# Kernel tuning notes

Hardware: AMD Instinct MI355X
Metric: run time of the kernel (lower is better)

The kernel has to match this reference:

```python
import jax, jax.numpy as jnp
import numpy as np

EPS = 1e-8

def real_sph_harm(u):
    # u: [..., 3] unit vectors; returns real spherical harmonics for degrees 0..3
    x, y, z = u[..., 0], u[..., 1], u[..., 2]
    x2, y2, z2 = x * x, y * y, z * z
    Y0 = 0.28209479 * jnp.ones_like(x)[..., None]                       # [..., 1]
    Y1 = 0.48860251 * jnp.stack([y, z, x], axis=-1)                     # [..., 3]
    Y2 = jnp.stack([
        1.09254843 * x * y,
        1.09254843 * y * z,
        0.31539157 * (3.0 * z2 - 1.0),
        1.09254843 * x * z,
        0.54627422 * (x2 - y2)], axis=-1)                               # [..., 5]
    Y3 = jnp.stack([
        0.59004359 * y * (3.0 * x2 - y2),
        2.89061144 * x * y * z,
        0.45704579 * y * (5.0 * z2 - 1.0),
        0.37317633 * z * (5.0 * z2 - 3.0),
        0.45704579 * x * (5.0 * z2 - 1.0),
        1.44530572 * z * (x2 - y2),
        0.59004359 * x * (x2 - 3.0 * y2)], axis=-1)                     # [..., 7]
    return [Y0, Y1, Y2, Y3]


def setup_inputs() -> dict:
    key = jax.random.key(0)
    ks = jax.random.split(key, 8)
    B, N, F_IN, C, L = 8, 256, 4, 32, 4
    F_OUT = L * C * 2  # 256
    D_OUT = 40
    H = 32  # radial MLP hidden
    s = 0.1
    return {
        "x": jax.random.normal(ks[0], (B, N, F_IN), jnp.float32),
        "Wq": jax.random.normal(ks[1], (F_IN, C), jnp.float32) * s,
        "Wk": jax.random.normal(ks[2], (F_IN, C), jnp.float32) * s,
        "Wv": jax.random.normal(ks[3], (L, F_IN, C), jnp.float32) * s,
        "Rw1": jax.random.normal(ks[4], (1, H), jnp.float32) * s,
        "Rb1": jnp.zeros((H,), jnp.float32),
        "Rw2": jax.random.normal(ks[5], (H, L * C), jnp.float32) * s,
        "Rb2": jnp.zeros((L * C,), jnp.float32),
        "fc1_w": jax.random.normal(ks[6], (F_OUT, F_OUT), jnp.float32) * s,
        "fc1_b": jnp.zeros((F_OUT,), jnp.float32),
        "ln_g": jnp.ones((F_OUT,), jnp.float32),
        "ln_b": jnp.zeros((F_OUT,), jnp.float32),
        "fc2_w": jax.random.normal(ks[7], (F_OUT, D_OUT), jnp.float32) * s,
        "fc2_b": jnp.zeros((D_OUT,), jnp.float32),
    }


def reference(x, Wq, Wk, Wv, Rw1, Rb1, Rw2, Rb2, fc1_w, fc1_b, ln_g, ln_b, fc2_w, fc2_b):
    B, N, _ = x.shape
    L, _, C = Wv.shape
    # --- basis and r (get_basis_and_r): all-pairs displacements from coords ---
    coords = x[..., :3]
    d = coords[:, None, :, :] - coords[:, :, None, :]          # [B, i, j, 3]
    r = jnp.sqrt(jnp.sum(d * d, axis=-1) + EPS)                # [B, i, j]
    u = d / r[..., None]
    Ys = real_sph_harm(u)                                      # list of [B,i,j,2l+1]
    # --- radial net: per-degree, per-channel radial weights ---
    h = jax.nn.relu(r[..., None] @ Rw1 + Rb1)                  # [B,i,j,H]
    R = (h @ Rw2 + Rb2).reshape(B, N, N, L, C)                 # [B,i,j,L,C]
    # --- SSO3Res: equivariant attention (degree-0 q/k, basis-weighted values) ---
    q = x @ Wq
    k = x @ Wk
    logits = jnp.einsum('bic,bjc->bij', q, k) / jnp.sqrt(jnp.asarray(C, x.dtype))
    alpha = jax.nn.softmax(logits, axis=-1)                    # [B,i,j]
    vals = jnp.einsum('bjf,lfc->lbjc', x, Wv)                  # [L,B,j,C]
    invs = []
    for l in range(L):
        # out_l[i,c,m] = sum_j alpha_ij * R_ij,c * Y_l,ij,m * v_j,c
        out_l = jnp.einsum('bij,bijc,bijm,bjc->bicm', alpha, R[..., l, :], Ys[l], vals[l])
        invs.append(jnp.sqrt(jnp.sum(out_l * out_l, axis=-1) + EPS))   # [B,i,C]
    inv = jnp.concatenate(invs, axis=-1)                       # [B, N, L*C]
    # --- invariant pooling: max + mean over points -> out fiber (L*C*2) ---
    pooled = jnp.concatenate([inv.max(axis=1), inv.mean(axis=1)], axis=-1)  # [B, 2*L*C]
    # --- FC head: Linear -> LayerNorm -> ReLU -> Linear ---
    h1 = pooled @ fc1_w + fc1_b
    mu = h1.mean(axis=-1, keepdims=True)
    var = h1.var(axis=-1, keepdims=True)
    h1 = (h1 - mu) / jnp.sqrt(var + 1e-5) * ln_g + ln_b
    h1 = jax.nn.relu(h1)
    return h1 @ fc2_w + fc2_b
```

## Files before the change

### kernel.cpp

```cpp
#include <hip/hip_runtime.h>
#include <hip/hip_bf16.h>

#define BB 8
#define NN 256
#define LC 128

typedef short short8 __attribute__((ext_vector_type(8)));
typedef float f32x4 __attribute__((ext_vector_type(4)));

union U8 { short8 s; unsigned u[4]; };

__device__ inline unsigned pkbf(float a, float b){
    __hip_bfloat162 h = __float22bfloat162_rn(make_float2(a, b));
    union { __hip_bfloat162 h2; unsigned u; } cv; cv.h2 = h; return cv.u;
}

__device__ inline void stage_aY(short* __restrict__ slab, int j, float a,
                                float dx, float dy, float dz, float r2)
{
    const float ir = rsqrtf(r2);
    const float ux = dx*ir, uy = dy*ir, uz = dz*ir;
    const float X2 = ux*ux, Y2 = uy*uy, Z2 = uz*uz;
    const float y0  = 0.28209479f;
    const float y1  = 0.48860251f*uy, y2 = 0.48860251f*uz, y3 = 0.48860251f*ux;
    const float y4  = 1.09254843f*ux*uy;
    const float y5  = 1.09254843f*uy*uz;
    const float y6  = 0.31539157f*(3.f*Z2 - 1.f);
    const float y7  = 1.09254843f*ux*uz;
    const float y8  = 0.54627422f*(X2 - Y2);
    const float y9  = 0.59004359f*uy*(3.f*X2 - Y2);
    const float y10 = 2.89061144f*ux*uy*uz;
    const float y11 = 0.45704579f*uy*(5.f*Z2 - 1.f);
    const float y12 = 0.37317633f*uz*(5.f*Z2 - 3.f);
    const float y13 = 0.45704579f*ux*(5.f*Z2 - 1.f);
    const float y14 = 1.44530572f*uz*(X2 - Y2);
    const float y15 = 0.59004359f*ux*(X2 - 3.f*Y2);
    #define ST2(mm, va, vb) { unsigned uu = pkbf((va)*a, (vb)*a); \
        slab[(mm)*264 + j] = (short)(uu & 0xffff); slab[(mm+1)*264 + j] = (short)(uu >> 16); }
    ST2(0,  y0,  y1)  ST2(2,  y2,  y3)
    ST2(4,  y4,  y5)  ST2(6,  y6,  y7)
    ST2(8,  y8,  y9)  ST2(10, y10, y11)
    ST2(12, y12, y13) ST2(14, y14, y15)
    #undef ST2
}

__global__ __launch_bounds__(256) void so3_main(
    const float* __restrict__ xg,
    const float* __restrict__ Wq,
    const float* __restrict__ Wk,
    const float* __restrict__ Wv,
    const float* __restrict__ Rw1,
    const float* __restrict__ Rb1,
    const float* __restrict__ Rw2,
    const float* __restrict__ Rb2,
    float* __restrict__ invg)
{
    const int tid = threadIdx.x;
    const int blk = blockIdx.x;
    const int b = blk >> 6;
    const int iq = blk & 63;
    const int rowbase = b * NN;
    const int lane = tid & 63;
    const int w = tid >> 6;
    const int n = lane & 15;
    const int g = lane >> 4;
    const int kbase = g * 8;
    const int i = iq*4 + w;

    __shared__ __align__(16) float xs[NN*4];
    __shared__ short xsbf[NN*4];
    __shared__ short aYs[4][16*264];
    __shared__ float asum[4][256];

    const float4 x4 = *(const float4*)&xg[(rowbase + tid)*4];
    *(float4*)&xs[tid*4] = x4;
    {
        uint2 xb;
        xb.x = pkbf(x4.x, x4.y);
        xb.y = pkbf(x4.z, x4.w);
        *(uint2*)&xsbf[tid*4] = xb;
    }
    const float4 xi = *(const float4*)&xg[(rowbase + i)*4];

    float md0, md1, md2, md3;
    {
        const int c = lane & 31;
        const float qc = xi.x*Wq[c] + xi.y*Wq[32+c] + xi.z*Wq[64+c] + xi.w*Wq[96+c];
        md0 = qc*Wk[c]; md1 = qc*Wk[32+c]; md2 = qc*Wk[64+c]; md3 = qc*Wk[96+c];
        #pragma unroll
        for (int off = 16; off >= 1; off >>= 1) {
            md0 += __shfl_xor(md0, off);
            md1 += __shfl_xor(md1, off);
            md2 += __shfl_xor(md2, off);
            md3 += __shfl_xor(md3, off);
        }
        const float lscale = 0.17677669529663687f;
        md0 *= lscale; md1 *= lscale; md2 *= lscale; md3 *= lscale;
    }

    __syncthreads();

    float r_reg[16], lgv[16];
    #pragma unroll
    for (int s = 0; s < 16; ++s) {
        const float4 xa = *(const float4*)&xs[(16*s + n)*4];
        const float ddx = xa.x - xi.x, ddy = xa.y - xi.y, ddz = xa.z - xi.z;
        const float r2 = ddx*ddx + ddy*ddy + ddz*ddz + 1e-8f;
        r_reg[s] = sqrtf(r2);
        lgv[s] = md0*xa.x + md1*xa.y + md2*xa.z + md3*xa.w;
    }

    float mx = lgv[0];
    #pragma unroll
    for (int s = 1; s < 16; ++s) mx = fmaxf(mx, lgv[s]);
    #pragma unroll
    for (int off = 1; off <= 8; off <<= 1) mx = fmaxf(mx, __shfl_xor(mx, off));
    float es = 0.f;
    float ev[16];
    #pragma unroll
    for (int s = 0; s < 16; ++s) { ev[s] = __expf(lgv[s] - mx); es += ev[s]; }
    #pragma unroll
    for (int off = 1; off <= 8; off <<= 1) es += __shfl_xor(es, off);
    const float invS = 1.0f / es;
    #pragma unroll
    for (int s = 0; s < 16; ++s) asum[w][16*s + n] = ev[s]*invS;

    asm volatile("s_waitcnt lgkmcnt(0)" ::: "memory");
    __builtin_amdgcn_sched_barrier(0);

    short* slab = &aYs[w][0];
    #pragma unroll
    for (int e = 0; e < 4; ++e) {
        const int j = 64*g + 16*e + n;
        const float a = asum[w][j];
        const float4 xa = *(const float4*)&xs[j*4];
        const float ddx = xa.x - xi.x, ddy = xa.y - xi.y, ddz = xa.z - xi.z;
        const float r2 = ddx*ddx + ddy*ddy + ddz*ddz + 1e-8f;
        stage_aY(slab, j, a, ddx, ddy, ddz, r2);
    }

    float rw1q[8], rb1q[8];
    #pragma unroll
    for (int q = 0; q < 8; ++q) { rw1q[q] = Rw1[kbase+q]; rb1q[q] = Rb1[kbase+q]; }

    asm volatile("s_waitcnt lgkmcnt(0)" ::: "memory");
    __builtin_amdgcn_sched_barrier(0);

    const int boff = n*264 + 4*g;
    const f32x4 vzero = {0.f, 0.f, 0.f, 0.f};

    #pragma unroll
    for (int h4 = 0; h4 < 2; ++h4) {
        short8 bfrag[4], bv[4];
        float rb2v[4];
        #pragma unroll
        for (int t4 = 0; t4 < 4; ++t4) {
            const int col = h4*64 + t4*16 + n;
            U8 bf;
            #pragma unroll
            for (int qq = 0; qq < 4; ++qq)
                bf.u[qq] = pkbf(Rw2[(kbase+2*qq)*LC + col], Rw2[(kbase+2*qq+1)*LC + col]);
            bfrag[t4] = bf.s;
            rb2v[t4] = Rb2[col];
            U8 z; z.u[0] = 0; z.u[1] = 0; z.u[2] = 0; z.u[3] = 0;
            if (g == 0) {
                const int l = (h4*64 + t4*16) >> 5;
                const int cc = (t4 & 1)*16 + n;
                z.u[0] = pkbf(Wv[l*128 + cc],      Wv[l*128 + 32 + cc]);
                z.u[1] = pkbf(Wv[l*128 + 64 + cc], Wv[l*128 + 96 + cc]);
            }
            bv[t4] = z.s;
        }

        f32x4 acc[4] = {};

        #pragma unroll
        for (int tt = 0; tt < 8; ++tt) {
            const int j0 = 32*tt;

            const uint2 blo = *(const uint2*)&slab[boff + j0];
            const uint2 bhi = *(const uint2*)&slab[boff + j0 + 16];
            U8 bf2;
            bf2.u[0] = blo.x; bf2.u[1] = blo.y; bf2.u[2] = bhi.x; bf2.u[3] = bhi.y;

            uint2 P[2][4];
            #pragma unroll
            for (int jh = 0; jh < 2; ++jh) {
                const float rj = r_reg[2*tt + jh];
                U8 af;
                #pragma unroll
                for (int qq = 0; qq < 4; ++qq) {
                    const float h0 = fmaxf(rj*rw1q[2*qq]   + rb1q[2*qq],   0.f);
                    const float h1 = fmaxf(rj*rw1q[2*qq+1] + rb1q[2*qq+1], 0.f);
                    af.u[qq] = pkbf(h0, h1);
                }
                U8 afV; afV.u[0] = 0; afV.u[1] = 0; afV.u[2] = 0; afV.u[3] = 0;
                if (g == 0) {
                    const uint2 xb = *(const uint2*)&xsbf[(j0 + 16*jh + n)*4];
                    afV.u[0] = xb.x; afV.u[1] = xb.y;
                }
                #pragma unroll
                for (int t4 = 0; t4 < 4; ++t4) {
                    f32x4 d  = __builtin_amdgcn_mfma_f32_16x16x32_bf16(af.s,  bfrag[t4], vzero, 0, 0, 0);
                    f32x4 vv = __builtin_amdgcn_mfma_f32_16x16x32_bf16(afV.s, bv[t4],    vzero, 0, 0, 0);
                    P[jh][t4].x = pkbf((d[0]+rb2v[t4])*vv[0], (d[1]+rb2v[t4])*vv[1]);
                    P[jh][t4].y = pkbf((d[2]+rb2v[t4])*vv[2], (d[3]+rb2v[t4])*vv[3]);
                }
            }

            #pragma unroll
            for (int t4 = 0; t4 < 4; ++t4) {
                U8 a2;
                a2.u[0] = P[0][t4].x; a2.u[1] = P[0][t4].y;
                a2.u[2] = P[1][t4].x; a2.u[3] = P[1][t4].y;
                acc[t4] = __builtin_amdgcn_mfma_f32_16x16x32_bf16(a2.s, bf2.s, acc[t4], 0, 0, 0);
            }
        }

        #pragma unroll
        for (int t4 = 0; t4 < 4; ++t4) {
            const int l = h4*2 + (t4 >> 1);
            const int lo = l*l, hi = l*l + 2*l;
            const bool valid = (n >= lo) && (n <= hi);
            f32x4 aq = acc[t4];
            float s0 = valid ? aq[0]*aq[0] : 0.f;
            float s1 = valid ? aq[1]*aq[1] : 0.f;
            float s2 = valid ? aq[2]*aq[2] : 0.f;
            float s3 = valid ? aq[3]*aq[3] : 0.f;
            #pragma unroll
            for (int off = 1; off <= 8; off <<= 1) {
                s0 += __shfl_xor(s0, off);
                s1 += __shfl_xor(s1, off);
                s2 += __shfl_xor(s2, off);
                s3 += __shfl_xor(s3, off);
            }
            const float sv = (n==0) ? s0 : ((n==1) ? s1 : ((n==2) ? s2 : s3));
            if (n < 4) asum[w][h4*64 + t4*16 + g*4 + n] = sv;
        }
    }

    asm volatile("s_waitcnt lgkmcnt(0)" ::: "memory");
    __builtin_amdgcn_sched_barrier(0);
    {
        const float v0 = asum[w][lane];
        const float v1 = asum[w][lane + 64];
        float* dst = &invg[(size_t)(rowbase + i)*LC];
        dst[lane]      = sqrtf(v0 + 1e-8f);
        dst[lane + 64] = sqrtf(v1 + 1e-8f);
    }
}

__global__ __launch_bounds__(1024) void so3_post(
    const float* __restrict__ invg,
    const float* __restrict__ fc1_w,
    const float* __restrict__ fc1_b,
    const float* __restrict__ ln_g,
    const float* __restrict__ ln_b,
    const float* __restrict__ fc2_w,
    const float* __restrict__ fc2_b,
    float* __restrict__ outg)
{
    const int b = blockIdx.x;
    const int t = threadIdx.x;
    __shared__ float pm[8][128], ps[8][128];
    __shared__ float pooled[256];
    __shared__ float pfc1[2][256];
    __shared__ float h1s[256];
    __shared__ float pf2[8][40];
    __shared__ float redA[4], redB[4];

    {
        const int ig = t >> 7, lc = t & 127;
        float mxv = -1e30f, sm = 0.f;
        for (int i2 = ig; i2 < NN; i2 += 8) {
            const float v = invg[(size_t)(b*NN + i2)*LC + lc];
            mxv = fmaxf(mxv, v);
            sm += v;
        }
        pm[ig][lc] = mxv; ps[ig][lc] = sm;
    }
    __syncthreads();
    if (t < 128) {
        float m0 = pm[0][t];
        #pragma unroll
        for (int k = 1; k < 8; ++k) m0 = fmaxf(m0, pm[k][t]);
        pooled[t] = m0;
    } else if (t < 256) {
        const int lc = t - 128;
        float s0 = ps[0][lc];
        #pragma unroll
        for (int k = 1; k < 8; ++k) s0 += ps[k][lc];
        pooled[t] = s0 * (1.f/256.f);
    }
    __syncthreads();

    if (t < 512) {
        const int o = t & 255, kh = t >> 8;
        float acc = 0.f;
        for (int k = kh*128; k < kh*128 + 128; ++k)
            acc += pooled[k] * fc1_w[k*256 + o];
        pfc1[kh][o] = acc;
    }
    __syncthreads();

    float hval = 0.f;
    if (t < 256) hval = pfc1[0][t] + pfc1[1][t] + fc1_b[t];

    const int lane = t & 63, wid = t >> 6;
    float s1 = (t < 256) ? hval : 0.f;
    float s2 = (t < 256) ? hval*hval : 0.f;
    #pragma unroll
    for (int off = 32; off >= 1; off >>= 1) {
        s1 += __shfl_xor(s1, off);
        s2 += __shfl_xor(s2, off);
    }
    if (lane == 0 && wid < 4) { redA[wid] = s1; redB[wid] = s2; }
    __syncthreads();
    s1 = redA[0]+redA[1]+redA[2]+redA[3];
    s2 = redB[0]+redB[1]+redB[2]+redB[3];
    if (t < 256) {
        const float mu = s1 * (1.f/256.f);
        const float var = s2 * (1.f/256.f) - mu*mu;
        float v = (hval - mu) * rsqrtf(var + 1e-5f) * ln_g[t] + ln_b[t];
        h1s[t] = fmaxf(v, 0.f);
    }
    __syncthreads();

    if (t < 320) {
        const int o = t % 40, ks = t / 40;
        float acc = 0.f;
        for (int k = ks*32; k < ks*32 + 32; ++k)
            acc += h1s[k] * fc2_w[k*40 + o];
        pf2[ks][o] = acc;
    }
    __syncthreads();
    if (t < 40) {
        float o = fc2_b[t];
        #pragma unroll
        for (int ks = 0; ks < 8; ++ks) o += pf2[ks][t];
        outg[b*40 + t] = o;
    }
}

extern "C" void kernel_launch(void* const* d_in, const int* in_sizes, int n_in,
                              void* d_out, int out_size, void* d_ws, size_t ws_size,
                              hipStream_t stream) {
    const float* x     = (const float*)d_in[0];
    const float* Wq    = (const float*)d_in[1];
    const float* Wk    = (const float*)d_in[2];
    const float* Wv    = (const float*)d_in[3];
    const float* Rw1   = (const float*)d_in[4];
    const float* Rb1   = (const float*)d_in[5];
    const float* Rw2   = (const float*)d_in[6];
    const float* Rb2   = (const float*)d_in[7];
    const float* fc1_w = (const float*)d_in[8];
    const float* fc1_b = (const float*)d_in[9];
    const float* ln_g  = (const float*)d_in[10];
    const float* ln_b  = (const float*)d_in[11];
    const float* fc2_w = (const float*)d_in[12];
    const float* fc2_b = (const float*)d_in[13];
    float* out = (float*)d_out;

    float* invg = (float*)d_ws;

    so3_main<<<BB*64, 256, 0, stream>>>(x, Wq, Wk, Wv, Rw1, Rb1, Rw2, Rb2, invg);
    so3_post<<<BB, 1024, 0, stream>>>(invg, fc1_w, fc1_b, ln_g, ln_b, fc2_w, fc2_b, out);
}
```

Before: 43.43 us.

## Split rows across wave pairs, prepack weights, pool via atomics

```diff
diff --git a/kernel.cpp b/kernel.cpp
--- a/kernel.cpp
+++ b/kernel.cpp
@@ -44,33 +44,67 @@
     #undef ST2
 }
 
+__global__ __launch_bounds__(256) void so3_init(
+    const float* __restrict__ Rw2,
+    const float* __restrict__ Wv,
+    float* __restrict__ pmaxg,
+    float* __restrict__ psumg,
+    short* __restrict__ RW2bf,
+    short* __restrict__ WvBbf)
+{
+    const int t = threadIdx.x;
+    #pragma unroll
+    for (int rr = 0; rr < 4; ++rr) {
+        pmaxg[rr*256 + t] = 0.f;
+        psumg[rr*256 + t] = 0.f;
+    }
+    {
+        const int col = t >> 1, kh = (t & 1) * 16;
+        unsigned uu[8];
+        #pragma unroll
+        for (int q = 0; q < 8; ++q)
+            uu[q] = pkbf(Rw2[(kh + 2*q)*LC + col], Rw2[(kh + 2*q + 1)*LC + col]);
+        *(uint4*)&RW2bf[col*32 + kh]     = make_uint4(uu[0], uu[1], uu[2], uu[3]);
+        *(uint4*)&RW2bf[col*32 + kh + 8] = make_uint4(uu[4], uu[5], uu[6], uu[7]);
+    }
+    if (t < 128) {
+        const int l = t >> 5, c = t & 31;
+        const unsigned a0 = pkbf(Wv[l*128 + c],      Wv[l*128 + 32 + c]);
+        const unsigned a1 = pkbf(Wv[l*128 + 64 + c], Wv[l*128 + 96 + c]);
+        *(uint2*)&WvBbf[t*4] = make_uint2(a0, a1);
+    }
+}
+
 __global__ __launch_bounds__(256) void so3_main(
     const float* __restrict__ xg,
     const float* __restrict__ Wq,
     const float* __restrict__ Wk,
-    const float* __restrict__ Wv,
     const float* __restrict__ Rw1,
     const float* __restrict__ Rb1,
-    const float* __restrict__ Rw2,
+    const short* __restrict__ RW2bf,
     const float* __restrict__ Rb2,
-    float* __restrict__ invg)
+    const short* __restrict__ WvBbf,
+    float* __restrict__ pmaxg,
+    float* __restrict__ psumg)
 {
     const int tid = threadIdx.x;
     const int blk = blockIdx.x;
-    const int b = blk >> 6;
-    const int iq = blk & 63;
+    const int b = blk >> 7;
+    const int i0 = (blk & 127) << 1;
     const int rowbase = b * NN;
     const int lane = tid & 63;
     const int w = tid >> 6;
+    const int iw = w >> 1;
+    const int h = w & 1;
     const int n = lane & 15;
     const int g = lane >> 4;
     const int kbase = g * 8;
-    const int i = iq*4 + w;
+    const int i = i0 + iw;
 
     __shared__ __align__(16) float xs[NN*4];
     __shared__ short xsbf[NN*4];
-    __shared__ short aYs[4][16*264];
-    __shared__ float asum[4][256];
+    __shared__ short slab2[2][16*264];
+    __shared__ float aex[2][NN];
 
     const float4 x4 = *(const float4*)&xg[(rowbase + tid)*4];
     *(float4*)&xs[tid*4] = x4;
@@ -115,143 +149,127 @@
     for (int s = 1; s < 16; ++s) mx = fmaxf(mx, lgv[s]);
     #pragma unroll
     for (int off = 1; off <= 8; off <<= 1) mx = fmaxf(mx, __shfl_xor(mx, off));
-    float es = 0.f;
-    float ev[16];
+    float ev[16], es = 0.f;
     #pragma unroll
     for (int s = 0; s < 16; ++s) { ev[s] = __expf(lgv[s] - mx); es += ev[s]; }
     #pragma unroll
     for (int off = 1; off <= 8; off <<= 1) es += __shfl_xor(es, off);
     const float invS = 1.0f / es;
     #pragma unroll
-    for (int s = 0; s < 16; ++s) asum[w][16*s + n] = ev[s]*invS;
+    for (int s = 0; s < 16; ++s) aex[iw][16*s + n] = ev[s]*invS;
 
     asm volatile("s_waitcnt lgkmcnt(0)" ::: "memory");
     __builtin_amdgcn_sched_barrier(0);
 
-    short* slab = &aYs[w][0];
-    #pragma unroll
-    for (int e = 0; e < 4; ++e) {
-        const int j = 64*g + 16*e + n;
-        const float a = asum[w][j];
+    short* sl = &slab2[iw][0];
+    #pragma unroll
+    for (int e = 0; e < 2; ++e) {
+        const int j = 128*h + 16*(2*g + e) + n;
+        const float a = aex[iw][j];
         const float4 xa = *(const float4*)&xs[j*4];
         const float ddx = xa.x - xi.x, ddy = xa.y - xi.y, ddz = xa.z - xi.z;
         const float r2 = ddx*ddx + ddy*ddy + ddz*ddz + 1e-8f;
-        stage_aY(slab, j, a, ddx, ddy, ddz, r2);
+        stage_aY(sl, j, a, ddx, ddy, ddz, r2);
     }
 
     float rw1q[8], rb1q[8];
     #pragma unroll
     for (int q = 0; q < 8; ++q) { rw1q[q] = Rw1[kbase+q]; rb1q[q] = Rb1[kbase+q]; }
 
-    asm volatile("s_waitcnt lgkmcnt(0)" ::: "memory");
-    __builtin_amdgcn_sched_barrier(0);
+    short8 bfrag[4], bv[4];
+    float rb2v[4];
+    #pragma unroll
+    for (int t4 = 0; t4 < 4; ++t4) {
+        const int col = h*64 + t4*16 + n;
+        bfrag[t4] = *(const short8*)&RW2bf[col*32 + kbase];
+        rb2v[t4] = Rb2[col];
+        U8 z; z.u[0] = 0; z.u[1] = 0; z.u[2] = 0; z.u[3] = 0;
+        if (g == 0) {
+            const uint2 f = *(const uint2*)&WvBbf[col*4];
+            z.u[0] = f.x; z.u[1] = f.y;
+        }
+        bv[t4] = z.s;
+    }
+
+    __syncthreads();
 
     const int boff = n*264 + 4*g;
     const f32x4 vzero = {0.f, 0.f, 0.f, 0.f};
-
-    #pragma unroll
-    for (int h4 = 0; h4 < 2; ++h4) {
-        short8 bfrag[4], bv[4];
-        float rb2v[4];
-        #pragma unroll
-        for (int t4 = 0; t4 < 4; ++t4) {
-            const int col = h4*64 + t4*16 + n;
-            U8 bf;
+    f32x4 acc[4] = {};
+
+    #pragma unroll
+    for (int tt = 0; tt < 8; ++tt) {
+        const int j0 = 32*tt;
+
+        const uint2 blo = *(const uint2*)&sl[boff + j0];
+        const uint2 bhi = *(const uint2*)&sl[boff + j0 + 16];
+        U8 bf2;
+        bf2.u[0] = blo.x; bf2.u[1] = blo.y; bf2.u[2] = bhi.x; bf2.u[3] = bhi.y;
+
+        uint2 P[2][4];
+        #pragma unroll
+        for (int jh = 0; jh < 2; ++jh) {
+            const float rj = r_reg[2*tt + jh];
+            U8 af;
             #pragma unroll
-            for (int qq = 0; qq < 4; ++qq)
-                bf.u[qq] = pkbf(Rw2[(kbase+2*qq)*LC + col], Rw2[(kbase+2*qq+1)*LC + col]);
-            bfrag[t4] = bf.s;
-            rb2v[t4] = Rb2[col];
-            U8 z; z.u[0] = 0; z.u[1] = 0; z.u[2] = 0; z.u[3] = 0;
+            for (int qq = 0; qq < 4; ++qq) {
+                const float h0 = fmaxf(rj*rw1q[2*qq]   + rb1q[2*qq],   0.f);
+                const float h1 = fmaxf(rj*rw1q[2*qq+1] + rb1q[2*qq+1], 0.f);
+                af.u[qq] = pkbf(h0, h1);
+            }
+            U8 afV; afV.u[0] = 0; afV.u[1] = 0; afV.u[2] = 0; afV.u[3] = 0;
             if (g == 0) {
-                const int l = (h4*64 + t4*16) >> 5;
-                const int cc = (t4 & 1)*16 + n;
-                z.u[0] = pkbf(Wv[l*128 + cc],      Wv[l*128 + 32 + cc]);
-                z.u[1] = pkbf(Wv[l*128 + 64 + cc], Wv[l*128 + 96 + cc]);
+                const uint2 xb = *(const uint2*)&xsbf[(j0 + 16*jh + n)*4];
+                afV.u[0] = xb.x; afV.u[1] = xb.y;
             }
-            bv[t4] = z.s;
-        }
-
-        f32x4 acc[4] = {};
-
-        #pragma unroll
-        for (int tt = 0; tt < 8; ++tt) {
-            const int j0 = 32*tt;
-
-            const uint2 blo = *(const uint2*)&slab[boff + j0];
-            const uint2 bhi = *(const uint2*)&slab[boff + j0 + 16];
-            U8 bf2;
-            bf2.u[0] = blo.x; bf2.u[1] = blo.y; bf2.u[2] = bhi.x; bf2.u[3] = bhi.y;
-
-            uint2 P[2][4];
-            #pragma unroll
-            for (int jh = 0; jh < 2; ++jh) {
-                const float rj = r_reg[2*tt + jh];
-                U8 af;
-                #pragma unroll
-                for (int qq = 0; qq < 4; ++qq) {
-                    const float h0 = fmaxf(rj*rw1q[2*qq]   + rb1q[2*qq],   0.f);
-                    const float h1 = fmaxf(rj*rw1q[2*qq+1] + rb1q[2*qq+1], 0.f);
-                    af.u[qq] = pkbf(h0, h1);
-                }
-                U8 afV; afV.u[0] = 0; afV.u[1] = 0; afV.u[2] = 0; afV.u[3] = 0;
-                if (g == 0) {
-                    const uint2 xb = *(const uint2*)&xsbf[(j0 + 16*jh + n)*4];
-                    afV.u[0] = xb.x; afV.u[1] = xb.y;
-                }
-                #pragma unroll
-                for (int t4 = 0; t4 < 4; ++t4) {
-                    f32x4 d  = __builtin_amdgcn_mfma_f32_16x16x32_bf16(af.s,  bfrag[t4], vzero, 0, 0, 0);
-                    f32x4 vv = __builtin_amdgcn_mfma_f32_16x16x32_bf16(afV.s, bv[t4],    vzero, 0, 0, 0);
-                    P[jh][t4].x = pkbf((d[0]+rb2v[t4])*vv[0], (d[1]+rb2v[t4])*vv[1]);
-                    P[jh][t4].y = pkbf((d[2]+rb2v[t4])*vv[2], (d[3]+rb2v[t4])*vv[3]);
-                }
-            }
-
             #pragma unroll
             for (int t4 = 0; t4 < 4; ++t4) {
-                U8 a2;
-                a2.u[0] = P[0][t4].x; a2.u[1] = P[0][t4].y;
-                a2.u[2] = P[1][t4].x; a2.u[3] = P[1][t4].y;
-                acc[t4] = __builtin_amdgcn_mfma_f32_16x16x32_bf16(a2.s, bf2.s, acc[t4], 0, 0, 0);
+                f32x4 d  = __builtin_amdgcn_mfma_f32_16x16x32_bf16(af.s,  bfrag[t4], vzero, 0, 0, 0);
+                f32x4 vv = __builtin_amdgcn_mfma_f32_16x16x32_bf16(afV.s, bv[t4],    vzero, 0, 0, 0);
+                P[jh][t4].x = pkbf((d[0]+rb2v[t4])*vv[0], (d[1]+rb2v[t4])*vv[1]);
+                P[jh][t4].y = pkbf((d[2]+rb2v[t4])*vv[2], (d[3]+rb2v[t4])*vv[3]);
             }
         }
 
         #pragma unroll
         for (int t4 = 0; t4 < 4; ++t4) {
-            const int l = h4*2 + (t4 >> 1);
-            const int lo = l*l, hi = l*l + 2*l;
-            const bool valid = (n >= lo) && (n <= hi);
-            f32x4 aq = acc[t4];
-            float s0 = valid ? aq[0]*aq[0] : 0.f;
-            float s1 = valid ? aq[1]*aq[1] : 0.f;
-            float s2 = valid ? aq[2]*aq[2] : 0.f;
-            float s3 = valid ? aq[3]*aq[3] : 0.f;
-            #pragma unroll
-            for (int off = 1; off <= 8; off <<= 1) {
-                s0 += __shfl_xor(s0, off);
-                s1 += __shfl_xor(s1, off);
-                s2 += __shfl_xor(s2, off);
-                s3 += __shfl_xor(s3, off);
-            }
-            const float sv = (n==0) ? s0 : ((n==1) ? s1 : ((n==2) ? s2 : s3));
-            if (n < 4) asum[w][h4*64 + t4*16 + g*4 + n] = sv;
-        }
-    }
-
-    asm volatile("s_waitcnt lgkmcnt(0)" ::: "memory");
-    __builtin_amdgcn_sched_barrier(0);
-    {
-        const float v0 = asum[w][lane];
-        const float v1 = asum[w][lane + 64];
-        float* dst = &invg[(size_t)(rowbase + i)*LC];
-        dst[lane]      = sqrtf(v0 + 1e-8f);
-        dst[lane + 64] = sqrtf(v1 + 1e-8f);
-    }
-}
-
-__global__ __launch_bounds__(1024) void so3_post(
-    const float* __restrict__ invg,
+            U8 a2;
+            a2.u[0] = P[0][t4].x; a2.u[1] = P[0][t4].y;
+            a2.u[2] = P[1][t4].x; a2.u[3] = P[1][t4].y;
+            acc[t4] = __builtin_amdgcn_mfma_f32_16x16x32_bf16(a2.s, bf2.s, acc[t4], 0, 0, 0);
+        }
+    }
+
+    #pragma unroll
+    for (int t4 = 0; t4 < 4; ++t4) {
+        const int l = h*2 + (t4 >> 1);
+        const int lo = l*l, hi = l*l + 2*l;
+        const bool valid = (n >= lo) && (n <= hi);
+        f32x4 aq = acc[t4];
+        float s0 = valid ? aq[0]*aq[0] : 0.f;
+        float s1 = valid ? aq[1]*aq[1] : 0.f;
+        float s2 = valid ? aq[2]*aq[2] : 0.f;
+        float s3 = valid ? aq[3]*aq[3] : 0.f;
+        #pragma unroll
+        for (int off = 1; off <= 8; off <<= 1) {
+            s0 += __shfl_xor(s0, off);
+            s1 += __shfl_xor(s1, off);
+            s2 += __shfl_xor(s2, off);
+            s3 += __shfl_xor(s3, off);
+        }
+        const float sv = (n==0) ? s0 : ((n==1) ? s1 : ((n==2) ? s2 : s3));
+        if (n < 4) {
+            const float v = sqrtf(sv + 1e-8f);
+            const int col = h*64 + t4*16 + g*4 + n;
+            atomicMax((unsigned*)&pmaxg[b*LC + col], __float_as_uint(v));
+            atomicAdd(&psumg[b*LC + col], v);
+        }
+    }
+}
+
+__global__ __launch_bounds__(512) void so3_post(
+    const float* __restrict__ pmaxg,
+    const float* __restrict__ psumg,
     const float* __restrict__ fc1_w,
     const float* __restrict__ fc1_b,
     const float* __restrict__ ln_g,
@@ -262,39 +280,17 @@
 {
     const int b = blockIdx.x;
     const int t = threadIdx.x;
-    __shared__ float pm[8][128], ps[8][128];
     __shared__ float pooled[256];
     __shared__ float pfc1[2][256];
     __shared__ float h1s[256];
     __shared__ float pf2[8][40];
-    __shared__ float redA[4], redB[4];
+    __shared__ float redA[8], redB[8];
+
+    if (t < 128)      pooled[t] = pmaxg[b*LC + t];
+    else if (t < 256) pooled[t] = psumg[b*LC + (t-128)] * (1.f/256.f);
+    __syncthreads();
 
     {
-        const int ig = t >> 7, lc = t & 127;
-        float mxv = -1e30f, sm = 0.f;
-        for (int i2 = ig; i2 < NN; i2 += 8) {
-            const float v = invg[(size_t)(b*NN + i2)*LC + lc];
-            mxv = fmaxf(mxv, v);
-            sm += v;
-        }
-        pm[ig][lc] = mxv; ps[ig][lc] = sm;
-    }
-    __syncthreads();
-    if (t < 128) {
-        float m0 = pm[0][t];
-        #pragma unroll
-        for (int k = 1; k < 8; ++k) m0 = fmaxf(m0, pm[k][t]);
-        pooled[t] = m0;
-    } else if (t < 256) {
-        const int lc = t - 128;
-        float s0 = ps[0][lc];
-        #pragma unroll
-        for (int k = 1; k < 8; ++k) s0 += ps[k][lc];
-        pooled[t] = s0 * (1.f/256.f);
-    }
-    __syncthreads();
-
-    if (t < 512) {
         const int o = t & 255, kh = t >> 8;
         float acc = 0.f;
         for (int k = kh*128; k < kh*128 + 128; ++k)
@@ -314,7 +310,7 @@
         s1 += __shfl_xor(s1, off);
         s2 += __shfl_xor(s2, off);
     }
-    if (lane == 0 && wid < 4) { redA[wid] = s1; redB[wid] = s2; }
+    if (lane == 0) { redA[wid] = s1; redB[wid] = s2; }
     __syncthreads();
     s1 = redA[0]+redA[1]+redA[2]+redA[3];
     s2 = redB[0]+redB[1]+redB[2]+redB[3];
@@ -361,8 +357,13 @@
     const float* fc2_b = (const float*)d_in[13];
     float* out = (float*)d_out;
 
-    float* invg = (float*)d_ws;
-
-    so3_main<<<BB*64, 256, 0, stream>>>(x, Wq, Wk, Wv, Rw1, Rb1, Rw2, Rb2, invg);
-    so3_post<<<BB, 1024, 0, stream>>>(invg, fc1_w, fc1_b, ln_g, ln_b, fc2_w, fc2_b, out);
-}
+    float* ws = (float*)d_ws;
+    float* pmaxg = ws;
+    float* psumg = pmaxg + BB*LC;
+    short* RW2bf = (short*)(psumg + BB*LC);
+    short* WvBbf = RW2bf + 4096;
+
+    so3_init<<<1, 256, 0, stream>>>(Rw2, Wv, pmaxg, psumg, RW2bf, WvBbf);
+    so3_main<<<BB*128, 256, 0, stream>>>(x, Wq, Wk, Rw1, Rb1, RW2bf, Rb2, WvBbf, pmaxg, psumg);
+    so3_post<<<BB, 512, 0, stream>>>(pmaxg, psumg, fc1_w, fc1_b, ln_g, ln_b, fc2_w, fc2_b, out);
+}
```

Result: slower. 50.97 us (+17.4%).

## Split each query row's neighbor range across two waves with cross-wave softmax and reduction

Applied to the files above, without the earlier changes.

```diff
diff --git a/kernel.cpp b/kernel.cpp
--- a/kernel.cpp
+++ b/kernel.cpp
@@ -4,6 +4,7 @@
 #define BB 8
 #define NN 256
 #define LC 128
+#define SSTR 136
 
 typedef short short8 __attribute__((ext_vector_type(8)));
 typedef float f32x4 __attribute__((ext_vector_type(4)));
@@ -15,7 +16,7 @@
     union { __hip_bfloat162 h2; unsigned u; } cv; cv.h2 = h; return cv.u;
 }
 
-__device__ inline void stage_aY(short* __restrict__ slab, int j, float a,
+__device__ inline void stage_aY(short* __restrict__ slab, int jj, float a,
                                 float dx, float dy, float dz, float r2)
 {
     const float ir = rsqrtf(r2);
@@ -36,7 +37,7 @@
     const float y14 = 1.44530572f*uz*(X2 - Y2);
     const float y15 = 0.59004359f*ux*(X2 - 3.f*Y2);
     #define ST2(mm, va, vb) { unsigned uu = pkbf((va)*a, (vb)*a); \
-        slab[(mm)*264 + j] = (short)(uu & 0xffff); slab[(mm+1)*264 + j] = (short)(uu >> 16); }
+        slab[(mm)*SSTR + jj] = (short)(uu & 0xffff); slab[(mm+1)*SSTR + jj] = (short)(uu >> 16); }
     ST2(0,  y0,  y1)  ST2(2,  y2,  y3)
     ST2(4,  y4,  y5)  ST2(6,  y6,  y7)
     ST2(8,  y8,  y9)  ST2(10, y10, y11)
@@ -57,20 +58,25 @@
 {
     const int tid = threadIdx.x;
     const int blk = blockIdx.x;
-    const int b = blk >> 6;
-    const int iq = blk & 63;
+    const int b = blk >> 7;
+    const int i0 = (blk & 127) << 1;
     const int rowbase = b * NN;
     const int lane = tid & 63;
     const int w = tid >> 6;
+    const int iw = w >> 1;
+    const int jh2 = w & 1;
+    const int pw = w ^ 1;
     const int n = lane & 15;
     const int g = lane >> 4;
     const int kbase = g * 8;
-    const int i = iq*4 + w;
+    const int i = i0 + iw;
+    const int jb = jh2 * 128;
 
     __shared__ __align__(16) float xs[NN*4];
     __shared__ short xsbf[NN*4];
-    __shared__ short aYs[4][16*264];
-    __shared__ float asum[4][256];
+    __shared__ __align__(8) short aYs[4][16*SSTR];
+    __shared__ float asum[4][128];
+    __shared__ float pex[4][2];
 
     const float4 x4 = *(const float4*)&xg[(rowbase + tid)*4];
     *(float4*)&xs[tid*4] = x4;
@@ -100,43 +106,50 @@
 
     __syncthreads();
 
-    float r_reg[16], lgv[16];
+    float r_reg[8], ev[8];
+    float mx;
+    {
+        float lgv[8];
+        #pragma unroll
+        for (int s = 0; s < 8; ++s) {
+            const float4 xa = *(const float4*)&xs[(jb + 16*s + n)*4];
+            const float ddx = xa.x - xi.x, ddy = xa.y - xi.y, ddz = xa.z - xi.z;
+            const float r2 = ddx*ddx + ddy*ddy + ddz*ddz + 1e-8f;
+            r_reg[s] = sqrtf(r2);
+            lgv[s] = md0*xa.x + md1*xa.y + md2*xa.z + md3*xa.w;
+        }
+        mx = lgv[0];
+        #pragma unroll
+        for (int s = 1; s < 8; ++s) mx = fmaxf(mx, lgv[s]);
+        #pragma unroll
+        for (int off = 1; off <= 8; off <<= 1) mx = fmaxf(mx, __shfl_xor(mx, off));
+        float es = 0.f;
+        #pragma unroll
+        for (int s = 0; s < 8; ++s) { ev[s] = __expf(lgv[s] - mx); es += ev[s]; }
+        #pragma unroll
+        for (int off = 1; off <= 8; off <<= 1) es += __shfl_xor(es, off);
+        if (lane == 0) { pex[w][0] = mx; pex[w][1] = es; }
+        #pragma unroll
+        for (int s = 0; s < 8; ++s) asum[w][16*s + n] = ev[s];
+    }
+
+    __syncthreads();
+
+    const float mxp = pex[pw][0], esp = pex[pw][1];
+    const float es  = pex[w][1];
+    const float M = fmaxf(mx, mxp);
+    const float S = es*__expf(mx - M) + esp*__expf(mxp - M);
+    const float scale = __expf(mx - M) / S;
+
+    short* slab = &aYs[w][0];
     #pragma unroll
-    for (int s = 0; s < 16; ++s) {
-        const float4 xa = *(const float4*)&xs[(16*s + n)*4];
+    for (int e = 0; e < 2; ++e) {
+        const int jj = 32*g + 16*e + n;
+        const float a = asum[w][jj] * scale;
+        const float4 xa = *(const float4*)&xs[(jb + jj)*4];
         const float ddx = xa.x - xi.x, ddy = xa.y - xi.y, ddz = xa.z - xi.z;
         const float r2 = ddx*ddx + ddy*ddy + ddz*ddz + 1e-8f;
-        r_reg[s] = sqrtf(r2);
-        lgv[s] = md0*xa.x + md1*xa.y + md2*xa.z + md3*xa.w;
-    }
-
-    float mx = lgv[0];
-    #pragma unroll
-    for (int s = 1; s < 16; ++s) mx = fmaxf(mx, lgv[s]);
-    #pragma unroll
-    for (int off = 1; off <= 8; off <<= 1) mx = fmaxf(mx, __shfl_xor(mx, off));
-    float es = 0.f;
-    float ev[16];
-    #pragma unroll
-    for (int s = 0; s < 16; ++s) { ev[s] = __expf(lgv[s] - mx); es += ev[s]; }
-    #pragma unroll
-    for (int off = 1; off <= 8; off <<= 1) es += __shfl_xor(es, off);
-    const float invS = 1.0f / es;
-    #pragma unroll
-    for (int s = 0; s < 16; ++s) asum[w][16*s + n] = ev[s]*invS;
-
-    asm volatile("s_waitcnt lgkmcnt(0)" ::: "memory");
-    __builtin_amdgcn_sched_barrier(0);
-
-    short* slab = &aYs[w][0];
-    #pragma unroll
-    for (int e = 0; e < 4; ++e) {
-        const int j = 64*g + 16*e + n;
-        const float a = asum[w][j];
-        const float4 xa = *(const float4*)&xs[j*4];
-        const float ddx = xa.x - xi.x, ddy = xa.y - xi.y, ddz = xa.z - xi.z;
-        const float r2 = ddx*ddx + ddy*ddy + ddz*ddz + 1e-8f;
-        stage_aY(slab, j, a, ddx, ddy, ddz, r2);
+        stage_aY(slab, jj, a, ddx, ddy, ddz, r2);
     }
 
     float rw1q[8], rb1q[8];
@@ -146,8 +159,9 @@
     asm volatile("s_waitcnt lgkmcnt(0)" ::: "memory");
     __builtin_amdgcn_sched_barrier(0);
 
-    const int boff = n*264 + 4*g;
+    const int boff = n*SSTR + 4*g;
     const f32x4 vzero = {0.f, 0.f, 0.f, 0.f};
+    f32x4 acc2[2][4] = {};
 
     #pragma unroll
     for (int h4 = 0; h4 < 2; ++h4) {
@@ -172,14 +186,12 @@
             bv[t4] = z.s;
         }
 
-        f32x4 acc[4] = {};
-
-        #pragma unroll
-        for (int tt = 0; tt < 8; ++tt) {
-            const int j0 = 32*tt;
-
-            const uint2 blo = *(const uint2*)&slab[boff + j0];
-            const uint2 bhi = *(const uint2*)&slab[boff + j0 + 16];
+        #pragma unroll
+        for (int tt = 0; tt < 4; ++tt) {
+            const int j0l = 32*tt;
+
+            const uint2 blo = *(const uint2*)&slab[boff + j0l];
+            const uint2 bhi = *(const uint2*)&slab[boff + j0l + 16];
             U8 bf2;
             bf2.u[0] = blo.x; bf2.u[1] = blo.y; bf2.u[2] = bhi.x; bf2.u[3] = bhi.y;
 
@@ -196,7 +208,7 @@
                 }
                 U8 afV; afV.u[0] = 0; afV.u[1] = 0; afV.u[2] = 0; afV.u[3] = 0;
                 if (g == 0) {
-                    const uint2 xb = *(const uint2*)&xsbf[(j0 + 16*jh + n)*4];
+                    const uint2 xb = *(const uint2*)&xsbf[(jb + j0l + 16*jh + n)*4];
                     afV.u[0] = xb.x; afV.u[1] = xb.y;
                 }
                 #pragma unroll
@@ -213,20 +225,39 @@
                 U8 a2;
                 a2.u[0] = P[0][t4].x; a2.u[1] = P[0][t4].y;
                 a2.u[2] = P[1][t4].x; a2.u[3] = P[1][t4].y;
-                acc[t4] = __builtin_amdgcn_mfma_f32_16x16x32_bf16(a2.s, bf2.s, acc[t4], 0, 0, 0);
-            }
-        }
-
+                acc2[h4][t4] = __builtin_amdgcn_mfma_f32_16x16x32_bf16(a2.s, bf2.s, acc2[h4][t4], 0, 0, 0);
+            }
+        }
+    }
+
+    asm volatile("s_waitcnt lgkmcnt(0)" ::: "memory");
+    __builtin_amdgcn_sched_barrier(0);
+    {
+        float* pacc = (float*)slab;
+        const int oh = 1 - jh2;
+        #pragma unroll
+        for (int t4 = 0; t4 < 4; ++t4)
+            #pragma unroll
+            for (int q = 0; q < 4; ++q)
+                pacc[(t4*4 + q)*64 + lane] = acc2[oh][t4][q];
+    }
+    __syncthreads();
+
+    {
+        const float* ppacc = (const float*)&aYs[pw][0];
         #pragma unroll
         for (int t4 = 0; t4 < 4; ++t4) {
-            const int l = h4*2 + (t4 >> 1);
+            const int l = jh2*2 + (t4 >> 1);
             const int lo = l*l, hi = l*l + 2*l;
             const bool valid = (n >= lo) && (n <= hi);
-            f32x4 aq = acc[t4];
-            float s0 = valid ? aq[0]*aq[0] : 0.f;
-            float s1 = valid ? aq[1]*aq[1] : 0.f;
-            float s2 = valid ? aq[2]*aq[2] : 0.f;
-            float s3 = valid ? aq[3]*aq[3] : 0.f;
+            float s0 = acc2[jh2][t4][0] + ppacc[(t4*4+0)*64 + lane];
+            float s1 = acc2[jh2][t4][1] + ppacc[(t4*4+1)*64 + lane];
+            float s2 = acc2[jh2][t4][2] + ppacc[(t4*4+2)*64 + lane];
+            float s3 = acc2[jh2][t4][3] + ppacc[(t4*4+3)*64 + lane];
+            s0 = valid ? s0*s0 : 0.f;
+            s1 = valid ? s1*s1 : 0.f;
+            s2 = valid ? s2*s2 : 0.f;
+            s3 = valid ? s3*s3 : 0.f;
             #pragma unroll
             for (int off = 1; off <= 8; off <<= 1) {
                 s0 += __shfl_xor(s0, off);
@@ -235,18 +266,11 @@
                 s3 += __shfl_xor(s3, off);
             }
             const float sv = (n==0) ? s0 : ((n==1) ? s1 : ((n==2) ? s2 : s3));
-            if (n < 4) asum[w][h4*64 + t4*16 + g*4 + n] = sv;
-        }
-    }
-
-    asm volatile("s_waitcnt lgkmcnt(0)" ::: "memory");
-    __builtin_amdgcn_sched_barrier(0);
-    {
-        const float v0 = asum[w][lane];
-        const float v1 = asum[w][lane + 64];
-        float* dst = &invg[(size_t)(rowbase + i)*LC];
-        dst[lane]      = sqrtf(v0 + 1e-8f);
-        dst[lane + 64] = sqrtf(v1 + 1e-8f);
+            if (n < 4) {
+                const int col = jh2*64 + t4*16 + g*4 + n;
+                invg[(size_t)(rowbase + i)*LC + col] = sqrtf(sv + 1e-8f);
+            }
+        }
     }
 }
 
@@ -363,6 +387,6 @@
 
     float* invg = (float*)d_ws;
 
-    so3_main<<<BB*64, 256, 0, stream>>>(x, Wq, Wk, Wv, Rw1, Rb1, Rw2, Rb2, invg);
+    so3_main<<<BB*128, 256, 0, stream>>>(x, Wq, Wk, Wv, Rw1, Rb1, Rw2, Rb2, invg);
     so3_post<<<BB, 1024, 0, stream>>>(invg, fc1_w, fc1_b, ln_g, ln_b, fc2_w, fc2_b, out);
 }
```

Measured after the change: 60.99 us. 1.4x slower.

## Split point pooling into separate multi-block kernel before FC head

Applied to the files above, without the earlier changes.

```diff
diff --git a/kernel.cpp b/kernel.cpp
--- a/kernel.cpp
+++ b/kernel.cpp
@@ -250,8 +250,30 @@
     }
 }
 
-__global__ __launch_bounds__(1024) void so3_post(
+__global__ __launch_bounds__(128) void so3_pool(
     const float* __restrict__ invg,
+    float* __restrict__ pmax_p,
+    float* __restrict__ psum_p)
+{
+    const int blk = blockIdx.x;
+    const int b = blk >> 3;
+    const int chunk = blk & 7;
+    const int t = threadIdx.x;
+    const int ibase = b*NN + chunk*32;
+    float mx = -1e30f, sm = 0.f;
+    #pragma unroll 4
+    for (int k = 0; k < 32; ++k) {
+        const float v = invg[(size_t)(ibase + k)*LC + t];
+        mx = fmaxf(mx, v);
+        sm += v;
+    }
+    pmax_p[(size_t)blk*LC + t] = mx;
+    psum_p[(size_t)blk*LC + t] = sm;
+}
+
+__global__ __launch_bounds__(512) void so3_post(
+    const float* __restrict__ pmax_p,
+    const float* __restrict__ psum_p,
     const float* __restrict__ fc1_w,
     const float* __restrict__ fc1_b,
     const float* __restrict__ ln_g,
@@ -262,39 +284,27 @@
 {
     const int b = blockIdx.x;
     const int t = threadIdx.x;
-    __shared__ float pm[8][128], ps[8][128];
     __shared__ float pooled[256];
     __shared__ float pfc1[2][256];
     __shared__ float h1s[256];
     __shared__ float pf2[8][40];
-    __shared__ float redA[4], redB[4];
-
-    {
-        const int ig = t >> 7, lc = t & 127;
-        float mxv = -1e30f, sm = 0.f;
-        for (int i2 = ig; i2 < NN; i2 += 8) {
-            const float v = invg[(size_t)(b*NN + i2)*LC + lc];
-            mxv = fmaxf(mxv, v);
-            sm += v;
-        }
-        pm[ig][lc] = mxv; ps[ig][lc] = sm;
-    }
-    __syncthreads();
+    __shared__ float redA[8], redB[8];
+
     if (t < 128) {
-        float m0 = pm[0][t];
-        #pragma unroll
-        for (int k = 1; k < 8; ++k) m0 = fmaxf(m0, pm[k][t]);
+        float m0 = pmax_p[(size_t)(b*8)*LC + t];
+        #pragma unroll
+        for (int k = 1; k < 8; ++k) m0 = fmaxf(m0, pmax_p[(size_t)(b*8 + k)*LC + t]);
         pooled[t] = m0;
     } else if (t < 256) {
         const int lc = t - 128;
-        float s0 = ps[0][lc];
-        #pragma unroll
-        for (int k = 1; k < 8; ++k) s0 += ps[k][lc];
+        float s0 = psum_p[(size_t)(b*8)*LC + lc];
+        #pragma unroll
+        for (int k = 1; k < 8; ++k) s0 += psum_p[(size_t)(b*8 + k)*LC + lc];
         pooled[t] = s0 * (1.f/256.f);
     }
     __syncthreads();
 
-    if (t < 512) {
+    {
         const int o = t & 255, kh = t >> 8;
         float acc = 0.f;
         for (int k = kh*128; k < kh*128 + 128; ++k)
@@ -314,7 +324,7 @@
         s1 += __shfl_xor(s1, off);
         s2 += __shfl_xor(s2, off);
     }
-    if (lane == 0 && wid < 4) { redA[wid] = s1; redB[wid] = s2; }
+    if (lane == 0) { redA[wid] = s1; redB[wid] = s2; }
     __syncthreads();
     s1 = redA[0]+redA[1]+redA[2]+redA[3];
     s2 = redB[0]+redB[1]+redB[2]+redB[3];
@@ -361,8 +371,12 @@
     const float* fc2_b = (const float*)d_in[13];
     float* out = (float*)d_out;
 
-    float* invg = (float*)d_ws;
+    float* ws = (float*)d_ws;
+    float* invg   = ws;
+    float* pmax_p = invg + BB*NN*LC;
+    float* psum_p = pmax_p + BB*8*LC;
 
     so3_main<<<BB*64, 256, 0, stream>>>(x, Wq, Wk, Wv, Rw1, Rb1, Rw2, Rb2, invg);
-    so3_post<<<BB, 1024, 0, stream>>>(invg, fc1_w, fc1_b, ln_g, ln_b, fc2_w, fc2_b, out);
-}
+    so3_pool<<<BB*8, 128, 0, stream>>>(invg, pmax_p, psum_p);
+    so3_post<<<BB, 512, 0, stream>>>(pmax_p, psum_p, fc1_w, fc1_b, ln_g, ln_b, fc2_w, fc2_b, out);
+}
```

After: 37.42 us. -13.8%, faster.
